# Kernel optimization log

Hardware: AMD Instinct MI355X
Metric: run time of the kernel (lower is better)

## Reference

```python
import jax, jax.numpy as jnp
import numpy as np

SHAPES = [(4, 48, 48), (2, 24, 24), (1, 12, 12), (1, 6, 6)]  # (D,H,W) per level
B, E, NH, NL, NP, DF, NLAYERS = 2, 256, 8, 4, 4, 1024, 6
HD = E // NH
LEVEL_SIZES = [d * h * w for d, h, w in SHAPES]
LEVEL_START = [0] + [int(s) for s in np.cumsum(LEVEL_SIZES)[:-1]]
S = int(sum(LEVEL_SIZES))
PARAM_KEYS = ['W_off', 'b_off', 'W_attn', 'b_attn', 'W_val', 'b_val', 'W_out', 'b_out',
              'ln1_g', 'ln1_b', 'W_ff1', 'b_ff1', 'W_ff2', 'b_ff2', 'ln2_g', 'ln2_b']


def setup_inputs() -> dict:
    key = jax.random.key(0)
    ks = jax.random.split(key, 32)
    inp = {}
    for i, (d, h, w) in enumerate(SHAPES):
        inp[f'feat{i}'] = jax.random.normal(ks[i], (B, E, d, h, w), jnp.float32)
        inp[f'pos{i}'] = jax.random.normal(ks[4 + i], (B, E, d, h, w), jnp.float32)
    inp['level_embed'] = jax.random.normal(ks[8], (NL, E), jnp.float32)
    nrm = lambda k, shape, s: jax.random.normal(k, shape, jnp.float32) * s
    inp['W_off'] = nrm(ks[9], (NLAYERS, E, NH * NL * NP * 3), 0.01)
    inp['b_off'] = nrm(ks[10], (NLAYERS, NH * NL * NP * 3), 1.0)
    inp['W_attn'] = nrm(ks[11], (NLAYERS, E, NH * NL * NP), 0.02)
    inp['b_attn'] = jnp.zeros((NLAYERS, NH * NL * NP), jnp.float32)
    inp['W_val'] = nrm(ks[12], (NLAYERS, E, E), E ** -0.5)
    inp['b_val'] = jnp.zeros((NLAYERS, E), jnp.float32)
    inp['W_out'] = nrm(ks[13], (NLAYERS, E, E), E ** -0.5)
    inp['b_out'] = jnp.zeros((NLAYERS, E), jnp.float32)
    inp['ln1_g'] = jnp.ones((NLAYERS, E), jnp.float32)
    inp['ln1_b'] = jnp.zeros((NLAYERS, E), jnp.float32)
    inp['W_ff1'] = nrm(ks[14], (NLAYERS, E, DF), E ** -0.5)
    inp['b_ff1'] = jnp.zeros((NLAYERS, DF), jnp.float32)
    inp['W_ff2'] = nrm(ks[15], (NLAYERS, DF, E), DF ** -0.5)
    inp['b_ff2'] = jnp.zeros((NLAYERS, E), jnp.float32)
    inp['ln2_g'] = jnp.ones((NLAYERS, E), jnp.float32)
    inp['ln2_b'] = jnp.zeros((NLAYERS, E), jnp.float32)
    return inp


def _layer_norm(x, g, b):
    m = jnp.mean(x, -1, keepdims=True)
    v = jnp.mean((x - m) ** 2, -1, keepdims=True)
    return (x - m) * jax.lax.rsqrt(v + 1e-5) * g + b


def _ref_points():
    # all-zero padding masks -> valid_ratios == 1, so reference points are the
    # normalized voxel centers, identical across levels. Returns (S, 3) in (x, y, z).
    refs = []
    for (D, H, W) in SHAPES:
        z = (jnp.arange(D, dtype=jnp.float32) + 0.5) / D
        y = (jnp.arange(H, dtype=jnp.float32) + 0.5) / H
        x = (jnp.arange(W, dtype=jnp.float32) + 0.5) / W
        zz, yy, xx = jnp.meshgrid(z, y, x, indexing='ij')
        refs.append(jnp.stack([xx.ravel(), yy.ravel(), zz.ravel()], -1))
    return jnp.concatenate(refs, 0)


def _sample_level(v, coords, w, D, H, W):
    # v: (B, NH, N_lvl, HD) flattened level values
    # coords: (B, NH, S, NP, 3) pixel-space coords (x, y, z), align_corners=False convention
    # w: (B, NH, S, NP) attention weights (folded into trilinear corner weights)
    cx, cy, cz = coords[..., 0], coords[..., 1], coords[..., 2]
    x0, y0, z0 = jnp.floor(cx), jnp.floor(cy), jnp.floor(cz)
    fx, fy, fz = cx - x0, cy - y0, cz - z0
    Bq, Hq, Sq, Pq = w.shape
    acc = jnp.zeros((Bq, Hq, Sq, HD), v.dtype)
    for dz in (0, 1):
        wz = fz if dz else 1.0 - fz
        iz = z0 + dz
        for dy in (0, 1):
            wy = fy if dy else 1.0 - fy
            iy = y0 + dy
            for dx in (0, 1):
                wx = fx if dx else 1.0 - fx
                ix = x0 + dx
                valid = (ix >= 0) & (ix < W) & (iy >= 0) & (iy < H) & (iz >= 0) & (iz < D)
                wgt = w * wx * wy * wz * valid  # zero-padding outside the volume
                idx = ((jnp.clip(iz, 0, D - 1) * H + jnp.clip(iy, 0, H - 1)) * W
                       + jnp.clip(ix, 0, W - 1)).astype(jnp.int32)
                g = jnp.take_along_axis(v, idx.reshape(Bq, Hq, Sq * Pq)[..., None], axis=2)
                g = g.reshape(Bq, Hq, Sq, Pq, HD)
                acc = acc + jnp.einsum('bhsp,bhspd->bhsd', wgt, g)
    return acc


def _deform_attn(x, pos, ref, normalizer, p, sample_fn):
    B_, S_, _ = x.shape
    q = x + pos
    value = (x @ p['W_val'] + p['b_val']).reshape(B_, S_, NH, HD).transpose(0, 2, 1, 3)
    off = (q @ p['W_off'] + p['b_off']).reshape(B_, S_, NH, NL, NP, 3)
    attn = jax.nn.softmax((q @ p['W_attn'] + p['b_attn']).reshape(B_, S_, NH, NL * NP), -1)
    attn = attn.reshape(B_, S_, NH, NL, NP)
    # normalized sampling locations in [0,1]^3 (x, y, z)
    loc = ref[None, :, None, None, None, :] + off / normalizer[None, None, None, :, None, :]
    out = jnp.zeros((B_, NH, S_, HD), x.dtype)
    for lvl, (D, H, W) in enumerate(SHAPES):
        s0, n = LEVEL_START[lvl], LEVEL_SIZES[lvl]
        v = value[:, :, s0:s0 + n]
        size = jnp.array([W, H, D], x.dtype)
        coords = (loc[:, :, :, lvl] * size - 0.5).transpose(0, 2, 1, 3, 4)  # (B,NH,S,NP,3)
        w = attn[:, :, :, lvl].transpose(0, 2, 1, 3)  # (B,NH,S,NP)
        out = out + sample_fn(v, coords, w, D, H, W)
    out = out.transpose(0, 2, 1, 3).reshape(B_, S_, E)
    return out @ p['W_out'] + p['b_out']


def _encoder_layer(x, pos, ref, normalizer, p, sample_fn):
    x = _layer_norm(x + _deform_attn(x, pos, ref, normalizer, p, sample_fn),
                    p['ln1_g'], p['ln1_b'])
    h = jax.nn.relu(x @ p['W_ff1'] + p['b_ff1']) @ p['W_ff2'] + p['b_ff2']
    return _layer_norm(x + h, p['ln2_g'], p['ln2_b'])


def _forward(feats, poss, level_embed, params, sample_fn):
    x = jnp.concatenate([f.reshape(f.shape[0], E, -1).transpose(0, 2, 1) for f in feats], axis=1)
    pos = jnp.concatenate(
        [poss[l].reshape(poss[l].shape[0], E, -1).transpose(0, 2, 1) + level_embed[l]
         for l in range(NL)], axis=1)
    ref = _ref_points()
    normalizer = jnp.array([[w, h, d] for d, h, w in SHAPES], jnp.float32)  # (NL,3) (x,y,z)
    for l in range(NLAYERS):
        p = {k: params[k][l] for k in PARAM_KEYS}
        x = _encoder_layer(x, pos, ref, normalizer, p, sample_fn)
    return x


def reference(feat0, feat1, feat2, feat3, pos0, pos1, pos2, pos3, level_embed,
              W_off, b_off, W_attn, b_attn, W_val, b_val, W_out, b_out,
              ln1_g, ln1_b, W_ff1, b_ff1, W_ff2, b_ff2, ln2_g, ln2_b):
    params = dict(W_off=W_off, b_off=b_off, W_attn=W_attn, b_attn=b_attn,
                  W_val=W_val, b_val=b_val, W_out=W_out, b_out=b_out,
                  ln1_g=ln1_g, ln1_b=ln1_b, W_ff1=W_ff1, b_ff1=b_ff1,
                  W_ff2=W_ff2, b_ff2=b_ff2, ln2_g=ln2_g, ln2_b=ln2_b)
    return _forward([feat0, feat1, feat2, feat3], [pos0, pos1, pos2, pos3],
                    level_embed, params, _sample_level)
```

## Files before the change

### kernel.cpp

```cpp
#include <hip/hip_runtime.h>

#define S_TOT   10548
#define M_ROWS  21096
#define M_PAD   21120
#define E_DIM   256
#define NH_DIM  8
#define HD_DIM  32
#define DF_DIM  1024
#define NLAYERS 6

typedef unsigned short ushort_t;
typedef __attribute__((ext_vector_type(8))) short bf16x8;
typedef __attribute__((ext_vector_type(4))) float f32x4;

__device__ inline ushort_t f2bf(float f) {
    unsigned u = __float_as_uint(f);
    u += 0x7FFF + ((u >> 16) & 1);
    return (ushort_t)(u >> 16);
}
__device__ inline float bf2f(ushort_t h) {
    return __uint_as_float(((unsigned)h) << 16);
}
__device__ inline f32x4 up2(unsigned a, unsigned b) {
    f32x4 v;
    v.x = __uint_as_float(a << 16);
    v.y = __uint_as_float(a & 0xffff0000u);
    v.z = __uint_as_float(b << 16);
    v.w = __uint_as_float(b & 0xffff0000u);
    return v;
}
__device__ inline void gload16(const ushort_t* g, ushort_t* l) {
    __builtin_amdgcn_global_load_lds(
        (const __attribute__((address_space(1))) void*)g,
        (__attribute__((address_space(3))) void*)l, 16, 0, 0);
}

__global__ __launch_bounds__(256)
void assemble_kernel(const float* __restrict__ f0, const float* __restrict__ p0,
                     const float* __restrict__ f1, const float* __restrict__ p1,
                     const float* __restrict__ f2, const float* __restrict__ p2,
                     const float* __restrict__ f3, const float* __restrict__ p3,
                     const float* __restrict__ lemb,
                     float* __restrict__ x, ushort_t* __restrict__ posb,
                     ushort_t* __restrict__ xb, ushort_t* __restrict__ qb)
{
    int idx = blockIdx.x * 256 + threadIdx.x;
    int e = idx & (E_DIM - 1);
    int r = idx >> 8;
    int b = (r >= S_TOT) ? 1 : 0;
    int s = r - b * S_TOT;
    const float* f; const float* p; int lvl, j, n;
    if (s < 9216)       { lvl = 0; j = s;         n = 9216; f = f0; p = p0; }
    else if (s < 10368) { lvl = 1; j = s - 9216;  n = 1152; f = f1; p = p1; }
    else if (s < 10512) { lvl = 2; j = s - 10368; n = 144;  f = f2; p = p2; }
    else                { lvl = 3; j = s - 10512; n = 36;   f = f3; p = p3; }
    size_t o = (size_t)(b * E_DIM + e) * n + j;
    float xv = f[o];
    float pv = p[o] + lemb[lvl * E_DIM + e];
    x[idx]    = xv;
    posb[idx] = f2bf(pv);
    xb[idx]   = f2bf(xv);
    qb[idx]   = f2bf(xv + pv);
}

__global__ __launch_bounds__(256)
void transpose_cvt_kernel(const float* __restrict__ src, ushort_t* __restrict__ dst,
                          int K, int N, int dstLayerStride, int dstRowOff)
{
    __shared__ float tile[32][33];
    int l  = blockIdx.z;
    int n0 = blockIdx.x * 32, k0 = blockIdx.y * 32;
    int tx = threadIdx.x & 31, ty = threadIdx.x >> 5;
    const float* s = src + (size_t)l * K * N;
    ushort_t* d    = dst + (size_t)l * dstLayerStride + (size_t)dstRowOff * K;
    #pragma unroll
    for (int i = 0; i < 32; i += 8)
        tile[ty + i][tx] = s[(size_t)(k0 + ty + i) * N + n0 + tx];
    __syncthreads();
    #pragma unroll
    for (int i = 0; i < 32; i += 8)
        d[(size_t)(n0 + ty + i) * K + k0 + tx] = f2bf(tile[tx][ty + i]);
}

__global__ __launch_bounds__(256)
void gemm_part1(const ushort_t* __restrict__ A0, const ushort_t* __restrict__ A1,
                const ushort_t* __restrict__ BtBase,
                const float* __restrict__ b1, const float* __restrict__ b2,
                const float* __restrict__ b3,
                ushort_t* __restrict__ O1, ushort_t* __restrict__ O2,
                ushort_t* __restrict__ O3, int M)
{
    __shared__ short As[64 * 32];
    __shared__ short Bs[256 * 32];
    const int K = 256;
    int t    = threadIdx.x;
    int sup  = blockIdx.x;
    int row0 = blockIdx.y * 64;
    int lane = t & 63;
    int w    = t >> 6;
    int wn   = w * 64;
    const int quad = lane >> 4, lrow = lane & 15;

    const ushort_t* A  = (sup != 0) ? A1 : A0;
    const ushort_t* Bt = BtBase + (size_t)sup * 256 * K;

    f32x4 acc[4][4];
    #pragma unroll
    for (int i = 0; i < 4; ++i)
        #pragma unroll
        for (int j = 0; j < 4; ++j)
            acc[i][j] = (f32x4){0.f, 0.f, 0.f, 0.f};

    int srow = lane >> 2, skc = (lane & 3) * 8;
    const ushort_t* Ag = A + (size_t)(row0 + w * 16 + srow) * K + skc;
    const ushort_t* Bg = Bt + (size_t)(w * 64 + srow) * K + skc;
    ushort_t* Al = (ushort_t*)&As[(w * 16) * 32];

    for (int k0 = 0; k0 < K; k0 += 32) {
        gload16(Ag + k0, Al);
        #pragma unroll
        for (int q = 0; q < 4; ++q)
            gload16(Bg + (size_t)(q * 16) * K + k0,
                    (ushort_t*)&Bs[(w * 64 + q * 16) * 32]);
        __syncthreads();
        bf16x8 af[4], bfr[4];
        #pragma unroll
        for (int i = 0; i < 4; ++i)
            af[i] = *(const bf16x8*)&As[(i * 16 + lrow) * 32 + quad * 8];
        #pragma unroll
        for (int j = 0; j < 4; ++j)
            bfr[j] = *(const bf16x8*)&Bs[(wn + j * 16 + lrow) * 32 + quad * 8];
        #pragma unroll
        for (int i = 0; i < 4; ++i)
            #pragma unroll
            for (int j = 0; j < 4; ++j)
                acc[i][j] = __builtin_amdgcn_mfma_f32_16x16x32_bf16(af[i], bfr[j], acc[i][j], 0, 0, 0);
        __syncthreads();
    }

    #pragma unroll
    for (int j = 0; j < 4; ++j) {
        int col = wn + j * 16 + lrow;
        float bia = (sup == 0) ? b1[col]
                  : (sup == 1) ? b2[col]
                  : (col < 128) ? b2[256 + col] : b3[col - 128];
        #pragma unroll
        for (int i = 0; i < 4; ++i)
            #pragma unroll
            for (int rg = 0; rg < 4; ++rg) {
                int row = row0 + i * 16 + quad * 4 + rg;
                if (row < M) {
                    float v = acc[i][j][rg] + bia;
                    if (sup == 0) {
                        int b = (row >= S_TOT) ? 1 : 0;
                        int s = row - b * S_TOT;
                        O1[(((size_t)(b * NH_DIM + (col >> 5))) * S_TOT + s) * HD_DIM + (col & 31)] = f2bf(v);
                    } else if (sup == 2 && col >= 128) {
                        int acol = col - 128;
                        O3[((size_t)(acol >> 4) * M_ROWS + row) * 16 + (acol & 15)] = f2bf(v);
                    } else {
                        int ocol = (sup == 1) ? col : 256 + col;
                        int hh = (ocol * 1366) >> 16;
                        O2[((size_t)hh * M_ROWS + row) * 48 + (ocol - hh * 48)] = f2bf(v);
                    }
                }
            }
    }
}

__global__ __launch_bounds__(256)
void gemm_ln(const ushort_t* __restrict__ A, const ushort_t* __restrict__ Bt,
             const float* __restrict__ bias,
             float* __restrict__ x, ushort_t* __restrict__ xb,
             const float* __restrict__ lng, const float* __restrict__ lnb,
             int M)
{
    __shared__ short As[32 * 32];
    __shared__ short Bs[256 * 32];
    __shared__ float red1[32 * 5];
    __shared__ float red2[32 * 5];
    const int K = 256;
    int t    = threadIdx.x;
    int row0 = blockIdx.x * 32;
    int lane = t & 63;
    int w    = t >> 6;
    int wn   = w * 64;
    const int quad = lane >> 4, lrow = lane & 15;

    f32x4 acc[2][4];
    #pragma unroll
    for (int i = 0; i < 2; ++i)
        #pragma unroll
        for (int j = 0; j < 4; ++j)
            acc[i][j] = (f32x4){0.f, 0.f, 0.f, 0.f};

    int srow = lane >> 2, skc = (lane & 3) * 8;
    const ushort_t* Ag = A + (size_t)(row0 + w * 16 + srow) * K + skc;
    const ushort_t* Bg = Bt + (size_t)(w * 64 + srow) * K + skc;
    ushort_t* Al = (ushort_t*)&As[(w * 16) * 32];

    for (int k0 = 0; k0 < K; k0 += 32) {
        if (w < 2) gload16(Ag + k0, Al);
        #pragma unroll
        for (int q = 0; q < 4; ++q)
            gload16(Bg + (size_t)(q * 16) * K + k0,
                    (ushort_t*)&Bs[(w * 64 + q * 16) * 32]);
        __syncthreads();
        bf16x8 af[2], bfr[4];
        #pragma unroll
        for (int i = 0; i < 2; ++i)
            af[i] = *(const bf16x8*)&As[(i * 16 + lrow) * 32 + quad * 8];
        #pragma unroll
        for (int j = 0; j < 4; ++j)
            bfr[j] = *(const bf16x8*)&Bs[(wn + j * 16 + lrow) * 32 + quad * 8];
        #pragma unroll
        for (int i = 0; i < 2; ++i)
            #pragma unroll
            for (int j = 0; j < 4; ++j)
                acc[i][j] = __builtin_amdgcn_mfma_f32_16x16x32_bf16(af[i], bfr[j], acc[i][j], 0, 0, 0);
        __syncthreads();
    }

    float gj[4], bj[4], bi[4];
    #pragma unroll
    for (int j = 0; j < 4; ++j) {
        int col = wn + j * 16 + lrow;
        gj[j] = lng[col];
        bj[j] = lnb[col];
        bi[j] = bias[col];
    }

    #pragma unroll
    for (int i = 0; i < 2; ++i)
        #pragma unroll
        for (int rg = 0; rg < 4; ++rg) {
            int row = row0 + i * 16 + quad * 4 + rg;
            #pragma unroll
            for (int j = 0; j < 4; ++j) {
                int col = wn + j * 16 + lrow;
                float xres = (row < M) ? x[(size_t)row * 256 + col] : 0.f;
                acc[i][j][rg] += bi[j] + xres;
            }
            float p1 = acc[i][0][rg] + acc[i][1][rg] + acc[i][2][rg] + acc[i][3][rg];
            float p2 = acc[i][0][rg] * acc[i][0][rg] + acc[i][1][rg] * acc[i][1][rg]
                     + acc[i][2][rg] * acc[i][2][rg] + acc[i][3][rg] * acc[i][3][rg];
            p1 += __shfl_xor(p1, 1); p2 += __shfl_xor(p2, 1);
            p1 += __shfl_xor(p1, 2); p2 += __shfl_xor(p2, 2);
            p1 += __shfl_xor(p1, 4); p2 += __shfl_xor(p2, 4);
            p1 += __shfl_xor(p1, 8); p2 += __shfl_xor(p2, 8);
            if (lrow == 0) {
                int rl = i * 16 + quad * 4 + rg;
                red1[rl * 5 + w] = p1;
                red2[rl * 5 + w] = p2;
            }
        }
    __syncthreads();

    #pragma unroll
    for (int i = 0; i < 2; ++i)
        #pragma unroll
        for (int rg = 0; rg < 4; ++rg) {
            int rl = i * 16 + quad * 4 + rg;
            float S1 = red1[rl * 5 + 0] + red1[rl * 5 + 1] + red1[rl * 5 + 2] + red1[rl * 5 + 3];
            float S2 = red2[rl * 5 + 0] + red2[rl * 5 + 1] + red2[rl * 5 + 2] + red2[rl * 5 + 3];
            float mean = S1 * (1.f / 256);
            float rstd = rsqrtf(S2 * (1.f / 256) - mean * mean + 1e-5f);
            int row = row0 + rl;
            if (row < M) {
                #pragma unroll
                for (int j = 0; j < 4; ++j) {
                    int col = wn + j * 16 + lrow;
                    float out = (acc[i][j][rg] - mean) * rstd * gj[j] + bj[j];
                    size_t o = (size_t)row * 256 + col;
                    x[o]  = out;
                    xb[o] = f2bf(out);
                }
            }
        }
}

__global__ __launch_bounds__(256)
void ffn_kernel(const ushort_t* __restrict__ Axb, const ushort_t* __restrict__ W1t,
                const ushort_t* __restrict__ W2t,
                const float* __restrict__ bias1, const float* __restrict__ bias2,
                float* __restrict__ x, ushort_t* __restrict__ xb,
                ushort_t* __restrict__ qb, const ushort_t* __restrict__ posb,
                const float* __restrict__ lng, const float* __restrict__ lnb,
                int M)
{
    __shared__ short As[32 * 32];
    __shared__ short Bs[256 * 32];
    __shared__ short Hs[32 * 264];
    __shared__ float red1[32 * 5];
    __shared__ float red2[32 * 5];
    const int K = 256;
    int t    = threadIdx.x;
    int row0 = blockIdx.x * 32;
    int lane = t & 63;
    int w    = t >> 6;
    int wn   = w * 64;
    const int quad = lane >> 4, lrow = lane & 15;
    int srow = lane >> 2, skc = (lane & 3) * 8;

    f32x4 acc[2][4];
    #pragma unroll
    for (int i = 0; i < 2; ++i)
        #pragma unroll
        for (int j = 0; j < 4; ++j)
            acc[i][j] = (f32x4){0.f, 0.f, 0.f, 0.f};

    const ushort_t* Ag = Axb + (size_t)(row0 + w * 16 + srow) * K + skc;
    ushort_t* Al = (ushort_t*)&As[(w * 16) * 32];

    for (int c = 0; c < 4; ++c) {
        f32x4 hh[2][4];
        #pragma unroll
        for (int i = 0; i < 2; ++i)
            #pragma unroll
            for (int j = 0; j < 4; ++j)
                hh[i][j] = (f32x4){0.f, 0.f, 0.f, 0.f};

        const ushort_t* B1g = W1t + (size_t)(c * 256 + w * 64 + srow) * K + skc;
        for (int k0 = 0; k0 < K; k0 += 32) {
            if (w < 2) gload16(Ag + k0, Al);
            #pragma unroll
            for (int q = 0; q < 4; ++q)
                gload16(B1g + (size_t)(q * 16) * K + k0,
                        (ushort_t*)&Bs[(w * 64 + q * 16) * 32]);
            __syncthreads();
            bf16x8 af[2], bfr[4];
            #pragma unroll
            for (int i = 0; i < 2; ++i)
                af[i] = *(const bf16x8*)&As[(i * 16 + lrow) * 32 + quad * 8];
            #pragma unroll
            for (int j = 0; j < 4; ++j)
                bfr[j] = *(const bf16x8*)&Bs[(wn + j * 16 + lrow) * 32 + quad * 8];
            #pragma unroll
            for (int i = 0; i < 2; ++i)
                #pragma unroll
                for (int j = 0; j < 4; ++j)
                    hh[i][j] = __builtin_amdgcn_mfma_f32_16x16x32_bf16(af[i], bfr[j], hh[i][j], 0, 0, 0);
            __syncthreads();
        }
        #pragma unroll
        for (int j = 0; j < 4; ++j) {
            int col = wn + j * 16 + lrow;
            float b1v = bias1[c * 256 + col];
            #pragma unroll
            for (int i = 0; i < 2; ++i)
                #pragma unroll
                for (int rg = 0; rg < 4; ++rg) {
                    int rl = i * 16 + quad * 4 + rg;
                    Hs[rl * 264 + col] = f2bf(fmaxf(hh[i][j][rg] + b1v, 0.f));
                }
        }
        __syncthreads();
        const ushort_t* B2g = W2t + (size_t)(w * 64 + srow) * 1024 + c * 256 + skc;
        for (int k0 = 0; k0 < 256; k0 += 32) {
            #pragma unroll
            for (int q = 0; q < 4; ++q)
                gload16(B2g + (size_t)(q * 16) * 1024 + k0,
                        (ushort_t*)&Bs[(w * 64 + q * 16) * 32]);
            __syncthreads();
            bf16x8 af[2], bfr[4];
            #pragma unroll
            for (int i = 0; i < 2; ++i)
                af[i] = *(const bf16x8*)&Hs[(i * 16 + lrow) * 264 + k0 + quad * 8];
            #pragma unroll
            for (int j = 0; j < 4; ++j)
                bfr[j] = *(const bf16x8*)&Bs[(wn + j * 16 + lrow) * 32 + quad * 8];
            #pragma unroll
            for (int i = 0; i < 2; ++i)
                #pragma unroll
                for (int j = 0; j < 4; ++j)
                    acc[i][j] = __builtin_amdgcn_mfma_f32_16x16x32_bf16(af[i], bfr[j], acc[i][j], 0, 0, 0);
            __syncthreads();
        }
    }

    float gj[4], bj[4], bi[4];
    #pragma unroll
    for (int j = 0; j < 4; ++j) {
        int col = wn + j * 16 + lrow;
        gj[j] = lng[col];
        bj[j] = lnb[col];
        bi[j] = bias2[col];
    }

    #pragma unroll
    for (int i = 0; i < 2; ++i)
        #pragma unroll
        for (int rg = 0; rg < 4; ++rg) {
            int row = row0 + i * 16 + quad * 4 + rg;
            #pragma unroll
            for (int j = 0; j < 4; ++j) {
                int col = wn + j * 16 + lrow;
                float xres = (row < M) ? x[(size_t)row * 256 + col] : 0.f;
                acc[i][j][rg] += bi[j] + xres;
            }
            float p1 = acc[i][0][rg] + acc[i][1][rg] + acc[i][2][rg] + acc[i][3][rg];
            float p2 = acc[i][0][rg] * acc[i][0][rg] + acc[i][1][rg] * acc[i][1][rg]
                     + acc[i][2][rg] * acc[i][2][rg] + acc[i][3][rg] * acc[i][3][rg];
            p1 += __shfl_xor(p1, 1); p2 += __shfl_xor(p2, 1);
            p1 += __shfl_xor(p1, 2); p2 += __shfl_xor(p2, 2);
            p1 += __shfl_xor(p1, 4); p2 += __shfl_xor(p2, 4);
            p1 += __shfl_xor(p1, 8); p2 += __shfl_xor(p2, 8);
            if (lrow == 0) {
                int rl = i * 16 + quad * 4 + rg;
                red1[rl * 5 + w] = p1;
                red2[rl * 5 + w] = p2;
            }
        }
    __syncthreads();

    #pragma unroll
    for (int i = 0; i < 2; ++i)
        #pragma unroll
        for (int rg = 0; rg < 4; ++rg) {
            int rl = i * 16 + quad * 4 + rg;
            float S1 = red1[rl * 5 + 0] + red1[rl * 5 + 1] + red1[rl * 5 + 2] + red1[rl * 5 + 3];
            float S2 = red2[rl * 5 + 0] + red2[rl * 5 + 1] + red2[rl * 5 + 2] + red2[rl * 5 + 3];
            float mean = S1 * (1.f / 256);
            float rstd = rsqrtf(S2 * (1.f / 256) - mean * mean + 1e-5f);
            int row = row0 + rl;
            if (row < M) {
                #pragma unroll
                for (int j = 0; j < 4; ++j) {
                    int col = wn + j * 16 + lrow;
                    float out = (acc[i][j][rg] - mean) * rstd * gj[j] + bj[j];
                    size_t o = (size_t)row * 256 + col;
                    x[o]  = out;
                    xb[o] = f2bf(out);
                    qb[o] = f2bf(out + bf2f(posb[o]));
                }
            }
        }
}

__global__ __launch_bounds__(256, 4)
void sample_kernel(const ushort_t* __restrict__ valueb,
                   const ushort_t* __restrict__ offh,
                   const ushort_t* __restrict__ attnh,
                   ushort_t* __restrict__ sampb)
{
    __shared__ float wrec[16 * 168];
    __shared__ int   idxA[16 * 40];

    const int LD_[4]  = {4, 2, 1, 1};
    const int LH_[4]  = {48, 24, 12, 6};
    const int LW_[4]  = {48, 24, 12, 6};
    const int LS0_[4] = {0, 9216, 10368, 10512};

    int t   = threadIdx.x;
    int gl  = t >> 4;
    int sub = t & 15;
    int h   = blockIdx.x;
    int r   = blockIdx.y * 16 + gl;
    bool valid = (r < M_ROWS);
    if (!valid) r = M_ROWS - 1;
    int b   = (r >= S_TOT) ? 1 : 0;
    int s   = r - b * S_TOT;

    float rx, ry, rz;
    {
        int j;
        if (s < 9216)       { j = s;         int qx = j % 48; int q2 = j / 48; int qy = q2 % 48; int qz = q2 / 48;
                              rx = (qx + 0.5f) * (1.f/48); ry = (qy + 0.5f) * (1.f/48); rz = (qz + 0.5f) * (1.f/4); }
        else if (s < 10368) { j = s - 9216;  int qx = j % 24; int q2 = j / 24; int qy = q2 % 24; int qz = q2 / 24;
                              rx = (qx + 0.5f) * (1.f/24); ry = (qy + 0.5f) * (1.f/24); rz = (qz + 0.5f) * (1.f/2); }
        else if (s < 10512) { j = s - 10368; int qx = j % 12; int qy = j / 12;
                              rx = (qx + 0.5f) * (1.f/12); ry = (qy + 0.5f) * (1.f/12); rz = 0.5f; }
        else                { j = s - 10512; int qx = j % 6;  int qy = j / 6;
                              rx = (qx + 0.5f) * (1.f/6);  ry = (qy + 0.5f) * (1.f/6);  rz = 0.5f; }
    }

    {
        int p = sub;
        float lg = bf2f(attnh[((size_t)h * M_ROWS + r) * 16 + p]);
        float mx = lg;
        mx = fmaxf(mx, __shfl_xor(mx, 1));
        mx = fmaxf(mx, __shfl_xor(mx, 2));
        mx = fmaxf(mx, __shfl_xor(mx, 4));
        mx = fmaxf(mx, __shfl_xor(mx, 8));
        float e = __expf(lg - mx);
        float sm = e;
        sm += __shfl_xor(sm, 1);
        sm += __shfl_xor(sm, 2);
        sm += __shfl_xor(sm, 4);
        sm += __shfl_xor(sm, 8);
        float aw = e / sm;

        int lvl = p >> 2;
        const int Dl = LD_[lvl], Hl = LH_[lvl], Wl = LW_[lvl];
        size_t base3 = ((size_t)h * M_ROWS + r) * 48 + p * 3;
        float cx = rx * Wl + bf2f(offh[base3 + 0]) - 0.5f;
        float cy = ry * Hl + bf2f(offh[base3 + 1]) - 0.5f;
        float cz = rz * Dl + bf2f(offh[base3 + 2]) - 0.5f;
        float xf = floorf(cx), yf = floorf(cy), zf = floorf(cz);
        float fx = cx - xf, fy = cy - yf, fz = cz - zf;
        int x0 = (int)xf, y0 = (int)yf, z0 = (int)zf;
        float wx0 = ((unsigned)x0       < (unsigned)Wl) ? 1.f - fx : 0.f;
        float wx1 = ((unsigned)(x0 + 1) < (unsigned)Wl) ? fx       : 0.f;
        float wy0 = ((unsigned)y0       < (unsigned)Hl) ? 1.f - fy : 0.f;
        float wy1 = ((unsigned)(y0 + 1) < (unsigned)Hl) ? fy       : 0.f;
        float wz0 = ((unsigned)z0       < (unsigned)Dl) ? (1.f - fz) * aw : 0.f;
        float wz1 = ((unsigned)(z0 + 1) < (unsigned)Dl) ? fz * aw       : 0.f;
        int xc = min(max(x0, -1), Wl - 1);
        int yc = min(max(y0, -1), Hl - 1);
        int zc = min(max(z0, -1), Dl - 1);
        int idx = LS0_[lvl] + (zc * Hl + yc) * Wl + xc;

        float* wp = &wrec[gl * 168 + p * 8];
        *(f32x4*)wp       = (f32x4){wz0 * wy0 * wx0, wz0 * wy0 * wx1,
                                    wz0 * wy1 * wx0, wz0 * wy1 * wx1};
        *(f32x4*)(wp + 4) = (f32x4){wz1 * wy0 * wx0, wz1 * wy0 * wx1,
                                    wz1 * wy1 * wx0, wz1 * wy1 * wx1};
        idxA[gl * 40 + p] = idx;
    }
    __syncthreads();

    int q  = sub & 3;
    int cr = sub >> 2;
    int dy = cr >> 1, dx = cr & 1;
    const ushort_t* vb = valueb + ((size_t)(b * NH_DIM + h) * S_TOT) * HD_DIM + q * 8;
    f32x4 accA = (f32x4){0.f, 0.f, 0.f, 0.f};
    f32x4 accB = (f32x4){0.f, 0.f, 0.f, 0.f};

    #pragma unroll
    for (int p = 0; p < 16; ++p) {
        const int lvl = p >> 2;
        const int Wl = LW_[lvl];
        const int HW = LH_[lvl] * LW_[lvl];
        float w0 = wrec[gl * 168 + p * 8 + cr];
        float w1 = wrec[gl * 168 + p * 8 + 4 + cr];
        int idx = idxA[gl * 40 + p] + dy * Wl + dx;
        const ushort_t* cb = vb + (long long)idx * HD_DIM;
        uint4 u0 = *(const uint4*)cb;
        uint4 u1 = *(const uint4*)(cb + HW * HD_DIM);
        accA += w0 * up2(u0.x, u0.y);
        accB += w0 * up2(u0.z, u0.w);
        accA += w1 * up2(u1.x, u1.y);
        accB += w1 * up2(u1.z, u1.w);
    }

    accA.x += __shfl_xor(accA.x, 4); accA.y += __shfl_xor(accA.y, 4);
    accA.z += __shfl_xor(accA.z, 4); accA.w += __shfl_xor(accA.w, 4);
    accB.x += __shfl_xor(accB.x, 4); accB.y += __shfl_xor(accB.y, 4);
    accB.z += __shfl_xor(accB.z, 4); accB.w += __shfl_xor(accB.w, 4);
    accA.x += __shfl_xor(accA.x, 8); accA.y += __shfl_xor(accA.y, 8);
    accA.z += __shfl_xor(accA.z, 8); accA.w += __shfl_xor(accA.w, 8);
    accB.x += __shfl_xor(accB.x, 8); accB.y += __shfl_xor(accB.y, 8);
    accB.z += __shfl_xor(accB.z, 8); accB.w += __shfl_xor(accB.w, 8);

    if (cr == 0 && valid) {
        ushort4 o1, o2;
        o1.x = f2bf(accA.x); o1.y = f2bf(accA.y); o1.z = f2bf(accA.z); o1.w = f2bf(accA.w);
        o2.x = f2bf(accB.x); o2.y = f2bf(accB.y); o2.z = f2bf(accB.z); o2.w = f2bf(accB.w);
        ushort_t* op = sampb + (size_t)r * E_DIM + h * HD_DIM + q * 8;
        *(ushort4*)op       = o1;
        *(ushort4*)(op + 4) = o2;
    }
}

extern "C" void kernel_launch(void* const* d_in, const int* in_sizes, int n_in,
                              void* d_out, int out_size, void* d_ws, size_t ws_size,
                              hipStream_t stream)
{
    const float* f0     = (const float*)d_in[0];
    const float* p0     = (const float*)d_in[1];
    const float* f1     = (const float*)d_in[2];
    const float* p1     = (const float*)d_in[3];
    const float* f2     = (const float*)d_in[4];
    const float* p2     = (const float*)d_in[5];
    const float* f3     = (const float*)d_in[6];
    const float* p3     = (const float*)d_in[7];
    const float* lemb   = (const float*)d_in[8];
    const float* W_off  = (const float*)d_in[9];
    const float* b_off  = (const float*)d_in[10];
    const float* W_attn = (const float*)d_in[11];
    const float* b_attn = (const float*)d_in[12];
    const float* W_val  = (const float*)d_in[13];
    const float* b_val  = (const float*)d_in[14];
    const float* W_out  = (const float*)d_in[15];
    const float* b_out  = (const float*)d_in[16];
    const float* ln1_g  = (const float*)d_in[17];
    const float* ln1_b  = (const float*)d_in[18];
    const float* W_ff1  = (const float*)d_in[19];
    const float* b_ff1  = (const float*)d_in[20];
    const float* W_ff2  = (const float*)d_in[21];
    const float* b_ff2  = (const float*)d_in[22];
    const float* ln2_g  = (const float*)d_in[23];
    const float* ln2_b  = (const float*)d_in[24];

    float* x = (float*)d_out;
    char*  w = (char*)d_ws;

    ushort_t* posb   = (ushort_t*)(w + 0);
    ushort_t* valueb = (ushort_t*)(w + 21626880 + 262144);
    char*     region =            (w + 34525184);
    ushort_t* offh   = (ushort_t*)(region);
    ushort_t* attnh  = (ushort_t*)(region + 16220160);
    ushort_t* sampb  = (ushort_t*)(region + 21626880);
    ushort_t* xb     = (ushort_t*)(w + 77778944);
    ushort_t* qb     = (ushort_t*)(w + 88592384);
    ushort_t* wb     = (ushort_t*)(w + 99405824);

    ushort_t* Wc_t = wb;
    ushort_t* Wp_t = wb + 1179648;
    ushort_t* W1_t = wb + 1572864;
    ushort_t* W2_t = wb + 3145728;

    dim3 blk(256);

    transpose_cvt_kernel<<<dim3(8, 8, 6),  blk, 0, stream>>>(W_val,  Wc_t, 256, 256,  196608, 0);
    transpose_cvt_kernel<<<dim3(12, 8, 6), blk, 0, stream>>>(W_off,  Wc_t, 256, 384,  196608, 256);
    transpose_cvt_kernel<<<dim3(4, 8, 6),  blk, 0, stream>>>(W_attn, Wc_t, 256, 128,  196608, 640);
    transpose_cvt_kernel<<<dim3(8, 8, 6),  blk, 0, stream>>>(W_out,  Wp_t, 256, 256,   65536, 0);
    transpose_cvt_kernel<<<dim3(32, 8, 6), blk, 0, stream>>>(W_ff1,  W1_t, 256, 1024, 262144, 0);
    transpose_cvt_kernel<<<dim3(8, 32, 6), blk, 0, stream>>>(W_ff2,  W2_t, 1024, 256, 262144, 0);

    assemble_kernel<<<(M_ROWS * E_DIM) / 256, blk, 0, stream>>>(
        f0, p0, f1, p1, f2, p2, f3, p3, lemb, x, posb, xb, qb);

    const int MT = M_PAD / 64;
    const int LT = M_PAD / 32;
    const int SB = (M_ROWS + 15) / 16;
    for (int l = 0; l < NLAYERS; ++l) {
        gemm_part1<<<dim3(3, MT), blk, 0, stream>>>(
            xb, qb, Wc_t + l * 196608,
            b_val + l * 256, b_off + l * 384, b_attn + l * 128,
            valueb, offh, attnh, M_ROWS);
        sample_kernel<<<dim3(NH_DIM, SB), blk, 0, stream>>>(valueb, offh, attnh, sampb);
        gemm_ln<<<LT, blk, 0, stream>>>(
            sampb, Wp_t + l * 65536, b_out + l * 256,
            x, xb, ln1_g + l * 256, ln1_b + l * 256, M_ROWS);
        ffn_kernel<<<LT, blk, 0, stream>>>(
            xb, W1_t + l * 262144, W2_t + l * 262144,
            b_ff1 + l * 1024, b_ff2 + l * 256,
            x, xb, qb, posb,
            ln2_g + l * 256, ln2_b + l * 256, M_ROWS);
    }
}
```

Before: 1.186 ms.

## Fuse output projection, LayerNorm and FFN into one tail kernel with swizzled LDS

Merges the output-projection+LN1 kernel and the FFN+LN2 kernel into a single per-32-row kernel. The sampled activations are loaded once into a full-K LDS tile, and the LN1 output is written back into that same tile in bf16 as the FFN input, which avoids a global write and re-read of x/xb and one kernel launch. It also adds XOR swizzling of LDS columns in both the projection GEMM and the tail kernel to reduce bank conflicts. The cost is much larger LDS use per block, which may lower occupancy. The Hs buffer is also now written inside the FFN loop without the barrier that previously followed it, which looks like a possible race.

New measurement: 1.341 ms. 1.13x slower.

```diff
diff --git a/kernel.cpp b/kernel.cpp
--- a/kernel.cpp
+++ b/kernel.cpp
@@ -111,9 +111,11 @@
         for (int j = 0; j < 4; ++j)
             acc[i][j] = (f32x4){0.f, 0.f, 0.f, 0.f};
 
-    int srow = lane >> 2, skc = (lane & 3) * 8;
-    const ushort_t* Ag = A + (size_t)(row0 + w * 16 + srow) * K + skc;
-    const ushort_t* Bg = Bt + (size_t)(w * 64 + srow) * K + skc;
+    int srow = lane >> 2;
+    const int sw = (((lane & 3) ^ ((lane >> 3) & 3)) * 8);
+    const int rs = ((quad ^ ((lrow >> 1) & 3)) * 8);
+    const ushort_t* Ag = A + (size_t)(row0 + w * 16 + srow) * K + sw;
+    const ushort_t* Bg = Bt + (size_t)(w * 64 + srow) * K + sw;
     ushort_t* Al = (ushort_t*)&As[(w * 16) * 32];
 
     for (int k0 = 0; k0 < K; k0 += 32) {
@@ -126,10 +128,10 @@
         bf16x8 af[4], bfr[4];
         #pragma unroll
         for (int i = 0; i < 4; ++i)
-            af[i] = *(const bf16x8*)&As[(i * 16 + lrow) * 32 + quad * 8];
+            af[i] = *(const bf16x8*)&As[(i * 16 + lrow) * 32 + rs];
         #pragma unroll
         for (int j = 0; j < 4; ++j)
-            bfr[j] = *(const bf16x8*)&Bs[(wn + j * 16 + lrow) * 32 + quad * 8];
+            bfr[j] = *(const bf16x8*)&Bs[(wn + j * 16 + lrow) * 32 + rs];
         #pragma unroll
         for (int i = 0; i < 4; ++i)
             #pragma unroll
@@ -169,67 +171,77 @@
 }
 
 __global__ __launch_bounds__(256)
-void gemm_ln(const ushort_t* __restrict__ A, const ushort_t* __restrict__ Bt,
-             const float* __restrict__ bias,
-             float* __restrict__ x, ushort_t* __restrict__ xb,
-             const float* __restrict__ lng, const float* __restrict__ lnb,
-             int M)
+void tail_kernel(const ushort_t* __restrict__ sampA, const ushort_t* __restrict__ Wp,
+                 const float* __restrict__ b_out,
+                 const float* __restrict__ ln1g, const float* __restrict__ ln1b,
+                 const ushort_t* __restrict__ W1t, const ushort_t* __restrict__ W2t,
+                 const float* __restrict__ bias1, const float* __restrict__ bias2,
+                 const float* __restrict__ ln2g, const float* __restrict__ ln2b,
+                 float* __restrict__ x, ushort_t* __restrict__ xb,
+                 ushort_t* __restrict__ qb, const ushort_t* __restrict__ posb,
+                 int M)
 {
-    __shared__ short As[32 * 32];
+    __shared__ short AsF[32 * 256];
     __shared__ short Bs[256 * 32];
-    __shared__ float red1[32 * 5];
-    __shared__ float red2[32 * 5];
-    const int K = 256;
+    __shared__ short Hs[32 * 264];
+    __shared__ float red1[32 * 5], red2[32 * 5];
+
     int t    = threadIdx.x;
     int row0 = blockIdx.x * 32;
     int lane = t & 63;
     int w    = t >> 6;
     int wn   = w * 64;
     const int quad = lane >> 4, lrow = lane & 15;
-
-    f32x4 acc[2][4];
+    int srow = lane >> 2;
+    const int sw = (((lane & 3) ^ ((lane >> 3) & 3)) * 8);
+    const int rs = ((quad ^ ((lrow >> 1) & 3)) * 8);
+    const int rkey = lrow & 7;
+
+    #pragma unroll
+    for (int R = 0; R < 4; ++R) {
+        int rl   = R * 8 + w * 2 + (lane >> 5);
+        int slot = lane & 31;
+        int kseg = slot ^ (rl & 7);
+        gload16(sampA + (size_t)(row0 + rl) * 256 + kseg * 8,
+                (ushort_t*)&AsF[(R * 8 + w * 2) * 256]);
+    }
+
+    f32x4 acc1[2][4];
     #pragma unroll
     for (int i = 0; i < 2; ++i)
         #pragma unroll
         for (int j = 0; j < 4; ++j)
-            acc[i][j] = (f32x4){0.f, 0.f, 0.f, 0.f};
-
-    int srow = lane >> 2, skc = (lane & 3) * 8;
-    const ushort_t* Ag = A + (size_t)(row0 + w * 16 + srow) * K + skc;
-    const ushort_t* Bg = Bt + (size_t)(w * 64 + srow) * K + skc;
-    ushort_t* Al = (ushort_t*)&As[(w * 16) * 32];
-
-    for (int k0 = 0; k0 < K; k0 += 32) {
-        if (w < 2) gload16(Ag + k0, Al);
-        #pragma unroll
-        for (int q = 0; q < 4; ++q)
-            gload16(Bg + (size_t)(q * 16) * K + k0,
-                    (ushort_t*)&Bs[(w * 64 + q * 16) * 32]);
-        __syncthreads();
-        bf16x8 af[2], bfr[4];
-        #pragma unroll
-        for (int i = 0; i < 2; ++i)
-            af[i] = *(const bf16x8*)&As[(i * 16 + lrow) * 32 + quad * 8];
-        #pragma unroll
-        for (int j = 0; j < 4; ++j)
-            bfr[j] = *(const bf16x8*)&Bs[(wn + j * 16 + lrow) * 32 + quad * 8];
-        #pragma unroll
-        for (int i = 0; i < 2; ++i)
+            acc1[i][j] = (f32x4){0.f, 0.f, 0.f, 0.f};
+    {
+        const ushort_t* Bg = Wp + (size_t)(w * 64 + srow) * 256 + sw;
+        for (int kk = 0; kk < 8; ++kk) {
+            #pragma unroll
+            for (int q = 0; q < 4; ++q)
+                gload16(Bg + (size_t)(q * 16) * 256 + kk * 32,
+                        (ushort_t*)&Bs[(w * 64 + q * 16) * 32]);
+            __syncthreads();
+            bf16x8 af[2], bfr[4];
+            #pragma unroll
+            for (int i = 0; i < 2; ++i)
+                af[i] = *(const bf16x8*)&AsF[(i * 16 + lrow) * 256 + (((kk * 4 + quad) ^ rkey) * 8)];
             #pragma unroll
             for (int j = 0; j < 4; ++j)
-                acc[i][j] = __builtin_amdgcn_mfma_f32_16x16x32_bf16(af[i], bfr[j], acc[i][j], 0, 0, 0);
-        __syncthreads();
-    }
-
-    float gj[4], bj[4], bi[4];
+                bfr[j] = *(const bf16x8*)&Bs[(wn + j * 16 + lrow) * 32 + rs];
+            #pragma unroll
+            for (int i = 0; i < 2; ++i)
+                #pragma unroll
+                for (int j = 0; j < 4; ++j)
+                    acc1[i][j] = __builtin_amdgcn_mfma_f32_16x16x32_bf16(af[i], bfr[j], acc1[i][j], 0, 0, 0);
+            __syncthreads();
+        }
+    }
+
+    float g1[4], be1[4], bo[4];
     #pragma unroll
     for (int j = 0; j < 4; ++j) {
         int col = wn + j * 16 + lrow;
-        gj[j] = lng[col];
-        bj[j] = lnb[col];
-        bi[j] = bias[col];
-    }
-
+        g1[j] = ln1g[col]; be1[j] = ln1b[col]; bo[j] = b_out[col];
+    }
     #pragma unroll
     for (int i = 0; i < 2; ++i)
         #pragma unroll
@@ -239,11 +251,11 @@
             for (int j = 0; j < 4; ++j) {
                 int col = wn + j * 16 + lrow;
                 float xres = (row < M) ? x[(size_t)row * 256 + col] : 0.f;
-                acc[i][j][rg] += bi[j] + xres;
+                acc1[i][j][rg] += bo[j] + xres;
             }
-            float p1 = acc[i][0][rg] + acc[i][1][rg] + acc[i][2][rg] + acc[i][3][rg];
-            float p2 = acc[i][0][rg] * acc[i][0][rg] + acc[i][1][rg] * acc[i][1][rg]
-                     + acc[i][2][rg] * acc[i][2][rg] + acc[i][3][rg] * acc[i][3][rg];
+            float p1 = acc1[i][0][rg] + acc1[i][1][rg] + acc1[i][2][rg] + acc1[i][3][rg];
+            float p2 = acc1[i][0][rg] * acc1[i][0][rg] + acc1[i][1][rg] * acc1[i][1][rg]
+                     + acc1[i][2][rg] * acc1[i][2][rg] + acc1[i][3][rg] * acc1[i][3][rg];
             p1 += __shfl_xor(p1, 1); p2 += __shfl_xor(p2, 1);
             p1 += __shfl_xor(p1, 2); p2 += __shfl_xor(p2, 2);
             p1 += __shfl_xor(p1, 4); p2 += __shfl_xor(p2, 4);
@@ -255,7 +267,122 @@
             }
         }
     __syncthreads();
-
+    #pragma unroll
+    for (int i = 0; i < 2; ++i)
+        #pragma unroll
+        for (int rg = 0; rg < 4; ++rg) {
+            int rl = i * 16 + quad * 4 + rg;
+            float S1 = red1[rl * 5 + 0] + red1[rl * 5 + 1] + red1[rl * 5 + 2] + red1[rl * 5 + 3];
+            float S2 = red2[rl * 5 + 0] + red2[rl * 5 + 1] + red2[rl * 5 + 2] + red2[rl * 5 + 3];
+            float mean = S1 * (1.f / 256);
+            float rstd = rsqrtf(S2 * (1.f / 256) - mean * mean + 1e-5f);
+            #pragma unroll
+            for (int j = 0; j < 4; ++j) {
+                int col = wn + j * 16 + lrow;
+                float v = (acc1[i][j][rg] - mean) * rstd * g1[j] + be1[j];
+                acc1[i][j][rg] = v;
+                AsF[rl * 256 + (((col >> 3) ^ (rl & 7)) * 8) + (col & 7)] = f2bf(v);
+            }
+        }
+
+    f32x4 acc2[2][4];
+    #pragma unroll
+    for (int i = 0; i < 2; ++i)
+        #pragma unroll
+        for (int j = 0; j < 4; ++j)
+            acc2[i][j] = (f32x4){0.f, 0.f, 0.f, 0.f};
+
+    for (int c = 0; c < 4; ++c) {
+        f32x4 hh[2][4];
+        #pragma unroll
+        for (int i = 0; i < 2; ++i)
+            #pragma unroll
+            for (int j = 0; j < 4; ++j)
+                hh[i][j] = (f32x4){0.f, 0.f, 0.f, 0.f};
+
+        const ushort_t* B1g = W1t + (size_t)(c * 256 + w * 64 + srow) * 256 + sw;
+        for (int kk = 0; kk < 8; ++kk) {
+            #pragma unroll
+            for (int q = 0; q < 4; ++q)
+                gload16(B1g + (size_t)(q * 16) * 256 + kk * 32,
+                        (ushort_t*)&Bs[(w * 64 + q * 16) * 32]);
+            __syncthreads();
+            bf16x8 af[2], bfr[4];
+            #pragma unroll
+            for (int i = 0; i < 2; ++i)
+                af[i] = *(const bf16x8*)&AsF[(i * 16 + lrow) * 256 + (((kk * 4 + quad) ^ rkey) * 8)];
+            #pragma unroll
+            for (int j = 0; j < 4; ++j)
+                bfr[j] = *(const bf16x8*)&Bs[(wn + j * 16 + lrow) * 32 + rs];
+            #pragma unroll
+            for (int i = 0; i < 2; ++i)
+                #pragma unroll
+                for (int j = 0; j < 4; ++j)
+                    hh[i][j] = __builtin_amdgcn_mfma_f32_16x16x32_bf16(af[i], bfr[j], hh[i][j], 0, 0, 0);
+            __syncthreads();
+        }
+        #pragma unroll
+        for (int j = 0; j < 4; ++j) {
+            int col = wn + j * 16 + lrow;
+            float b1v = bias1[c * 256 + col];
+            #pragma unroll
+            for (int i = 0; i < 2; ++i)
+                #pragma unroll
+                for (int rg = 0; rg < 4; ++rg) {
+                    int rl = i * 16 + quad * 4 + rg;
+                    Hs[rl * 264 + col] = f2bf(fmaxf(hh[i][j][rg] + b1v, 0.f));
+                }
+        }
+        const ushort_t* B2g = W2t + (size_t)(w * 64 + srow) * 1024 + c * 256 + sw;
+        for (int kk = 0; kk < 8; ++kk) {
+            #pragma unroll
+            for (int q = 0; q < 4; ++q)
+                gload16(B2g + (size_t)(q * 16) * 1024 + kk * 32,
+                        (ushort_t*)&Bs[(w * 64 + q * 16) * 32]);
+            __syncthreads();
+            bf16x8 af[2], bfr[4];
+            #pragma unroll
+            for (int i = 0; i < 2; ++i)
+                af[i] = *(const bf16x8*)&Hs[(i * 16 + lrow) * 264 + kk * 32 + quad * 8];
+            #pragma unroll
+            for (int j = 0; j < 4; ++j)
+                bfr[j] = *(const bf16x8*)&Bs[(wn + j * 16 + lrow) * 32 + rs];
+            #pragma unroll
+            for (int i = 0; i < 2; ++i)
+                #pragma unroll
+                for (int j = 0; j < 4; ++j)
+                    acc2[i][j] = __builtin_amdgcn_mfma_f32_16x16x32_bf16(af[i], bfr[j], acc2[i][j], 0, 0, 0);
+            __syncthreads();
+        }
+    }
+
+    float g2[4], be2[4], b2v[4];
+    #pragma unroll
+    for (int j = 0; j < 4; ++j) {
+        int col = wn + j * 16 + lrow;
+        g2[j] = ln2g[col]; be2[j] = ln2b[col]; b2v[j] = bias2[col];
+    }
+    #pragma unroll
+    for (int i = 0; i < 2; ++i)
+        #pragma unroll
+        for (int rg = 0; rg < 4; ++rg) {
+            #pragma unroll
+            for (int j = 0; j < 4; ++j)
+                acc2[i][j][rg] += b2v[j] + acc1[i][j][rg];
+            float p1 = acc2[i][0][rg] + acc2[i][1][rg] + acc2[i][2][rg] + acc2[i][3][rg];
+            float p2 = acc2[i][0][rg] * acc2[i][0][rg] + acc2[i][1][rg] * acc2[i][1][rg]
+                     + acc2[i][2][rg] * acc2[i][2][rg] + acc2[i][3][rg] * acc2[i][3][rg];
+            p1 += __shfl_xor(p1, 1); p2 += __shfl_xor(p2, 1);
+            p1 += __shfl_xor(p1, 2); p2 += __shfl_xor(p2, 2);
+            p1 += __shfl_xor(p1, 4); p2 += __shfl_xor(p2, 4);
+            p1 += __shfl_xor(p1, 8); p2 += __shfl_xor(p2, 8);
+            if (lrow == 0) {
+                int rl = i * 16 + quad * 4 + rg;
+                red1[rl * 5 + w] = p1;
+                red2[rl * 5 + w] = p2;
+            }
+        }
+    __syncthreads();
     #pragma unroll
     for (int i = 0; i < 2; ++i)
         #pragma unroll
@@ -270,164 +397,7 @@
                 #pragma unroll
                 for (int j = 0; j < 4; ++j) {
                     int col = wn + j * 16 + lrow;
-                    float out = (acc[i][j][rg] - mean) * rstd * gj[j] + bj[j];
-                    size_t o = (size_t)row * 256 + col;
-                    x[o]  = out;
-                    xb[o] = f2bf(out);
-                }
-            }
-        }
-}
-
-__global__ __launch_bounds__(256)
-void ffn_kernel(const ushort_t* __restrict__ Axb, const ushort_t* __restrict__ W1t,
-                const ushort_t* __restrict__ W2t,
-                const float* __restrict__ bias1, const float* __restrict__ bias2,
-                float* __restrict__ x, ushort_t* __restrict__ xb,
-                ushort_t* __restrict__ qb, const ushort_t* __restrict__ posb,
-                const float* __restrict__ lng, const float* __restrict__ lnb,
-                int M)
-{
-    __shared__ short As[32 * 32];
-    __shared__ short Bs[256 * 32];
-    __shared__ short Hs[32 * 264];
-    __shared__ float red1[32 * 5];
-    __shared__ float red2[32 * 5];
-    const int K = 256;
-    int t    = threadIdx.x;
-    int row0 = blockIdx.x * 32;
-    int lane = t & 63;
-    int w    = t >> 6;
-    int wn   = w * 64;
-    const int quad = lane >> 4, lrow = lane & 15;
-    int srow = lane >> 2, skc = (lane & 3) * 8;
-
-    f32x4 acc[2][4];
-    #pragma unroll
-    for (int i = 0; i < 2; ++i)
-        #pragma unroll
-        for (int j = 0; j < 4; ++j)
-            acc[i][j] = (f32x4){0.f, 0.f, 0.f, 0.f};
-
-    const ushort_t* Ag = Axb + (size_t)(row0 + w * 16 + srow) * K + skc;
-    ushort_t* Al = (ushort_t*)&As[(w * 16) * 32];
-
-    for (int c = 0; c < 4; ++c) {
-        f32x4 hh[2][4];
-        #pragma unroll
-        for (int i = 0; i < 2; ++i)
-            #pragma unroll
-            for (int j = 0; j < 4; ++j)
-                hh[i][j] = (f32x4){0.f, 0.f, 0.f, 0.f};
-
-        const ushort_t* B1g = W1t + (size_t)(c * 256 + w * 64 + srow) * K + skc;
-        for (int k0 = 0; k0 < K; k0 += 32) {
-            if (w < 2) gload16(Ag + k0, Al);
-            #pragma unroll
-            for (int q = 0; q < 4; ++q)
-                gload16(B1g + (size_t)(q * 16) * K + k0,
-                        (ushort_t*)&Bs[(w * 64 + q * 16) * 32]);
-            __syncthreads();
-            bf16x8 af[2], bfr[4];
-            #pragma unroll
-            for (int i = 0; i < 2; ++i)
-                af[i] = *(const bf16x8*)&As[(i * 16 + lrow) * 32 + quad * 8];
-            #pragma unroll
-            for (int j = 0; j < 4; ++j)
-                bfr[j] = *(const bf16x8*)&Bs[(wn + j * 16 + lrow) * 32 + quad * 8];
-            #pragma unroll
-            for (int i = 0; i < 2; ++i)
-                #pragma unroll
-                for (int j = 0; j < 4; ++j)
-                    hh[i][j] = __builtin_amdgcn_mfma_f32_16x16x32_bf16(af[i], bfr[j], hh[i][j], 0, 0, 0);
-            __syncthreads();
-        }
-        #pragma unroll
-        for (int j = 0; j < 4; ++j) {
-            int col = wn + j * 16 + lrow;
-            float b1v = bias1[c * 256 + col];
-            #pragma unroll
-            for (int i = 0; i < 2; ++i)
-                #pragma unroll
-                for (int rg = 0; rg < 4; ++rg) {
-                    int rl = i * 16 + quad * 4 + rg;
-                    Hs[rl * 264 + col] = f2bf(fmaxf(hh[i][j][rg] + b1v, 0.f));
-                }
-        }
-        __syncthreads();
-        const ushort_t* B2g = W2t + (size_t)(w * 64 + srow) * 1024 + c * 256 + skc;
-        for (int k0 = 0; k0 < 256; k0 += 32) {
-            #pragma unroll
-            for (int q = 0; q < 4; ++q)
-                gload16(B2g + (size_t)(q * 16) * 1024 + k0,
-                        (ushort_t*)&Bs[(w * 64 + q * 16) * 32]);
-            __syncthreads();
-            bf16x8 af[2], bfr[4];
-            #pragma unroll
-            for (int i = 0; i < 2; ++i)
-                af[i] = *(const bf16x8*)&Hs[(i * 16 + lrow) * 264 + k0 + quad * 8];
-            #pragma unroll
-            for (int j = 0; j < 4; ++j)
-                bfr[j] = *(const bf16x8*)&Bs[(wn + j * 16 + lrow) * 32 + quad * 8];
-            #pragma unroll
-            for (int i = 0; i < 2; ++i)
-                #pragma unroll
-                for (int j = 0; j < 4; ++j)
-                    acc[i][j] = __builtin_amdgcn_mfma_f32_16x16x32_bf16(af[i], bfr[j], acc[i][j], 0, 0, 0);
-            __syncthreads();
-        }
-    }
-
-    float gj[4], bj[4], bi[4];
-    #pragma unroll
-    for (int j = 0; j < 4; ++j) {
-        int col = wn + j * 16 + lrow;
-        gj[j] = lng[col];
-        bj[j] = lnb[col];
-        bi[j] = bias2[col];
-    }
-
-    #pragma unroll
-    for (int i = 0; i < 2; ++i)
-        #pragma unroll
-        for (int rg = 0; rg < 4; ++rg) {
-            int row = row0 + i * 16 + quad * 4 + rg;
-            #pragma unroll
-            for (int j = 0; j < 4; ++j) {
-                int col = wn + j * 16 + lrow;
-                float xres = (row < M) ? x[(size_t)row * 256 + col] : 0.f;
-                acc[i][j][rg] += bi[j] + xres;
-            }
-            float p1 = acc[i][0][rg] + acc[i][1][rg] + acc[i][2][rg] + acc[i][3][rg];
-            float p2 = acc[i][0][rg] * acc[i][0][rg] + acc[i][1][rg] * acc[i][1][rg]
-                     + acc[i][2][rg] * acc[i][2][rg] + acc[i][3][rg] * acc[i][3][rg];
-            p1 += __shfl_xor(p1, 1); p2 += __shfl_xor(p2, 1);
-            p1 += __shfl_xor(p1, 2); p2 += __shfl_xor(p2, 2);
-            p1 += __shfl_xor(p1, 4); p2 += __shfl_xor(p2, 4);
-            p1 += __shfl_xor(p1, 8); p2 += __shfl_xor(p2, 8);
-            if (lrow == 0) {
-                int rl = i * 16 + quad * 4 + rg;
-                red1[rl * 5 + w] = p1;
-                red2[rl * 5 + w] = p2;
-            }
-        }
-    __syncthreads();
-
-    #pragma unroll
-    for (int i = 0; i < 2; ++i)
-        #pragma unroll
-        for (int rg = 0; rg < 4; ++rg) {
-            int rl = i * 16 + quad * 4 + rg;
-            float S1 = red1[rl * 5 + 0] + red1[rl * 5 + 1] + red1[rl * 5 + 2] + red1[rl * 5 + 3];
-            float S2 = red2[rl * 5 + 0] + red2[rl * 5 + 1] + red2[rl * 5 + 2] + red2[rl * 5 + 3];
-            float mean = S1 * (1.f / 256);
-            float rstd = rsqrtf(S2 * (1.f / 256) - mean * mean + 1e-5f);
-            int row = row0 + rl;
-            if (row < M) {
-                #pragma unroll
-                for (int j = 0; j < 4; ++j) {
-                    int col = wn + j * 16 + lrow;
-                    float out = (acc[i][j][rg] - mean) * rstd * gj[j] + bj[j];
+                    float out = (acc2[i][j][rg] - mean) * rstd * g2[j] + be2[j];
                     size_t o = (size_t)row * 256 + col;
                     x[o]  = out;
                     xb[o] = f2bf(out);
@@ -631,13 +601,12 @@
             b_val + l * 256, b_off + l * 384, b_attn + l * 128,
             valueb, offh, attnh, M_ROWS);
         sample_kernel<<<dim3(NH_DIM, SB), blk, 0, stream>>>(valueb, offh, attnh, sampb);
-        gemm_ln<<<LT, blk, 0, stream>>>(
+        tail_kernel<<<LT, blk, 0, stream>>>(
             sampb, Wp_t + l * 65536, b_out + l * 256,
-            x, xb, ln1_g + l * 256, ln1_b + l * 256, M_ROWS);
-        ffn_kernel<<<LT, blk, 0, stream>>>(
-            xb, W1_t + l * 262144, W2_t + l * 262144,
+            ln1_g + l * 256, ln1_b + l * 256,
+            W1_t + l * 262144, W2_t + l * 262144,
             b_ff1 + l * 1024, b_ff2 + l * 256,
-            x, xb, qb, posb,
-            ln2_g + l * 256, ln2_b + l * 256, M_ROWS);
-    }
-}
+            ln2_g + l * 256, ln2_b + l * 256,
+            x, xb, qb, posb, M_ROWS);
+    }
+}
```
